# Performance work log

Measured on AMD Instinct MI355X. Metric: run time of the kernel, lower is better.

## Reference

```python
import jax, jax.numpy as jnp
import numpy as np

D_MODEL = 1024
NUM_HEADS = 16
D_K = D_MODEL // NUM_HEADS


def setup_inputs() -> dict:
    key = jax.random.key(0)
    ks = jax.random.split(key, 5)
    B, S = 4, 2048
    scale = 1.0 / np.sqrt(D_MODEL)
    x = jax.random.normal(ks[0], (B, S, D_MODEL), dtype=jnp.float32)
    Wq = jax.random.normal(ks[1], (D_MODEL, D_MODEL), dtype=jnp.float32) * scale
    Wk = jax.random.normal(ks[2], (D_MODEL, D_MODEL), dtype=jnp.float32) * scale
    Wv = jax.random.normal(ks[3], (D_MODEL, D_MODEL), dtype=jnp.float32) * scale
    Wo = jax.random.normal(ks[4], (D_MODEL, D_MODEL), dtype=jnp.float32) * scale
    return {"x": x, "Wq": Wq, "Wk": Wk, "Wv": Wv, "Wo": Wo}


def reference(x, Wq, Wk, Wv, Wo):
    B, S, _ = x.shape
    # projections (torch Linear: y = x @ W^T, no bias)
    def proj(W):
        y = jnp.einsum('bsd,ed->bse', x, W)
        # split heads: (b, s, h*dk) -> (b, h, s, dk)
        return y.reshape(B, S, NUM_HEADS, D_K).transpose(0, 2, 1, 3)
    Q, K, V = proj(Wq), proj(Wk), proj(Wv)
    scores = jnp.einsum('bhqd,bhkd->bhqk', Q, K) / np.sqrt(D_K)
    causal = jnp.tril(jnp.ones((S, S), dtype=bool))
    scores = jnp.where(causal, scores, -jnp.inf)
    attn = jax.nn.softmax(scores, axis=-1)
    out = jnp.einsum('bhqk,bhkd->bhqd', attn, V)
    out = out.transpose(0, 2, 1, 3).reshape(B, S, D_MODEL)
    return jnp.einsum('bse,de->bsd', out, Wo)
```

## Files before the change

kernel.cpp:

```cpp
#include <hip/hip_runtime.h>
#include <hip/hip_bf16.h>

typedef __attribute__((ext_vector_type(8))) short short8;
typedef __attribute__((ext_vector_type(4))) float f32x4;

static constexpr int DM = 1024;
static constexpr int NH = 16;
static constexpr int DK = 64;
static constexpr int SL = 2048;
static constexpr int BB = 4;
static constexpr size_t QKV_ELEMS = (size_t)BB * NH * SL * DK;
static constexpr float NEG_BIG = -30000.0f;
static constexpr float SC_LOG2E = 0.125f * 1.44269504088896340736f;

union PackB { __hip_bfloat16 h[8]; uint4 u; };
union Pack4 { __hip_bfloat16 h[4]; uint2 u; };

typedef __attribute__((address_space(1))) unsigned int gu32;
typedef __attribute__((address_space(3))) unsigned int lu32;
__device__ __forceinline__ void async_copy16(const void* g, void* l) {
    __builtin_amdgcn_global_load_lds((gu32*)g, (lu32*)l, 16, 0, 0);
}

__global__ __launch_bounds__(256)
void cvt_all(const float* __restrict__ x,
             const float* __restrict__ wq, const float* __restrict__ wk,
             const float* __restrict__ wv, const float* __restrict__ wo,
             __hip_bfloat16* __restrict__ dst)
{
    const size_t i = (size_t)blockIdx.x * 256 + threadIdx.x;
    const float* src; size_t local;
    if (i < 2097152) { src = x; local = i; }
    else {
        const size_t j = i - 2097152;
        const int r = (int)(j >> 18);
        local = j & 262143;
        src = (r == 0) ? wq : (r == 1) ? wk : (r == 2) ? wv : wo;
    }
    float4 f = reinterpret_cast<const float4*>(src)[local];
    Pack4 p;
    p.h[0] = __float2bfloat16(f.x); p.h[1] = __float2bfloat16(f.y);
    p.h[2] = __float2bfloat16(f.z); p.h[3] = __float2bfloat16(f.w);
    reinterpret_cast<uint2*>(dst)[i] = p.u;
}

__global__ __launch_bounds__(256)
void gemm_qkv(const __hip_bfloat16* __restrict__ A,
              const __hip_bfloat16* __restrict__ W,
              __hip_bfloat16* __restrict__ q_out,
              __hip_bfloat16* __restrict__ k_out,
              __hip_bfloat16* __restrict__ v_out)
{
    __shared__ __hip_bfloat16 As[128 * 32];
    __shared__ __hip_bfloat16 Bs[128 * 32];
    const int tid  = threadIdx.x;
    const int m0   = blockIdx.x * 128;
    const int n0   = blockIdx.y * 128;
    const int w    = tid >> 6;
    const int lane = tid & 63;
    const int quad = lane >> 4;
    const int ln   = lane & 15;
    const int wm   = (w & 1) * 64;
    const int wn   = (w >> 1) * 64;
    const int srow   = lane >> 2;
    const int schunk = (lane & 3) * 8;

    f32x4 acc[4][4] = {};

    for (int k0 = 0; k0 < DM; k0 += 32) {
        #pragma unroll
        for (int j = 0; j < 2; j++) {
            const int rbase = w * 32 + j * 16;
            async_copy16(A + (size_t)(m0 + rbase + srow) * DM + k0 + schunk,
                         &As[rbase * 32]);
            async_copy16(W + (size_t)(n0 + rbase + srow) * DM + k0 + schunk,
                         &Bs[rbase * 32]);
        }
        __syncthreads();

        short8 a[4], b[4];
        #pragma unroll
        for (int i = 0; i < 4; i++)
            a[i] = *reinterpret_cast<const short8*>(&As[(wm + i*16 + ln) * 32 + quad*8]);
        #pragma unroll
        for (int j = 0; j < 4; j++)
            b[j] = *reinterpret_cast<const short8*>(&Bs[(wn + j*16 + ln) * 32 + quad*8]);
        #pragma unroll
        for (int i = 0; i < 4; i++)
            #pragma unroll
            for (int j = 0; j < 4; j++)
                acc[i][j] = __builtin_amdgcn_mfma_f32_16x16x32_bf16(a[i], b[j], acc[i][j], 0, 0, 0);
        __syncthreads();
    }

    #pragma unroll
    for (int i = 0; i < 4; i++) {
        #pragma unroll
        for (int j = 0; j < 4; j++) {
            #pragma unroll
            for (int r = 0; r < 4; r++) {
                const int m = m0 + wm + i*16 + quad*4 + r;
                const int n = n0 + wn + j*16 + ln;
                const int b_ = m >> 11;
                const int s  = m & 2047;
                const int which = n >> 10;
                const int nn = n & 1023;
                const int h  = nn >> 6;
                const int d  = nn & 63;
                const __hip_bfloat16 v = __float2bfloat16(acc[i][j][r]);
                if (which == 0)
                    q_out[((size_t)((b_*NH + h)*SL + s))*DK + d] = v;
                else if (which == 1)
                    k_out[((size_t)((b_*NH + h)*SL + s))*DK + d] = v;
                else
                    v_out[((size_t)((b_*NH + h)*DK + d))*SL + s] = v;
            }
        }
    }
}

__global__ __launch_bounds__(256)
void gemm_wo(const __hip_bfloat16* __restrict__ A,
             const __hip_bfloat16* __restrict__ W,
             float* __restrict__ outp)
{
    __shared__ __hip_bfloat16 As[128 * 32];
    __shared__ __hip_bfloat16 Bs[128 * 32];
    const int tid  = threadIdx.x;
    const int m0   = blockIdx.x * 128;
    const int n0   = blockIdx.y * 128;
    const int w    = tid >> 6;
    const int lane = tid & 63;
    const int quad = lane >> 4;
    const int ln   = lane & 15;
    const int wm   = (w & 1) * 64;
    const int wn   = (w >> 1) * 64;
    const int srow   = lane >> 2;
    const int schunk = (lane & 3) * 8;

    f32x4 acc[4][4] = {};

    for (int k0 = 0; k0 < DM; k0 += 32) {
        #pragma unroll
        for (int j = 0; j < 2; j++) {
            const int rbase = w * 32 + j * 16;
            async_copy16(A + (size_t)(m0 + rbase + srow) * DM + k0 + schunk,
                         &As[rbase * 32]);
            async_copy16(W + (size_t)(n0 + rbase + srow) * DM + k0 + schunk,
                         &Bs[rbase * 32]);
        }
        __syncthreads();

        short8 a[4], b[4];
        #pragma unroll
        for (int i = 0; i < 4; i++)
            a[i] = *reinterpret_cast<const short8*>(&As[(wm + i*16 + ln) * 32 + quad*8]);
        #pragma unroll
        for (int j = 0; j < 4; j++)
            b[j] = *reinterpret_cast<const short8*>(&Bs[(wn + j*16 + ln) * 32 + quad*8]);
        #pragma unroll
        for (int i = 0; i < 4; i++)
            #pragma unroll
            for (int j = 0; j < 4; j++)
                acc[i][j] = __builtin_amdgcn_mfma_f32_16x16x32_bf16(a[i], b[j], acc[i][j], 0, 0, 0);
        __syncthreads();
    }

    #pragma unroll
    for (int i = 0; i < 4; i++)
        #pragma unroll
        for (int j = 0; j < 4; j++)
            #pragma unroll
            for (int r = 0; r < 4; r++) {
                const int m = m0 + wm + i*16 + quad*4 + r;
                const int n = n0 + wn + j*16 + ln;
                outp[(size_t)m * DM + n] = acc[i][j][r];
            }
}

template<bool A_BF16, int MODE>
__global__ __launch_bounds__(256)
void gemm_bt(const void* __restrict__ Ap,
             const float* __restrict__ W,
             void* __restrict__ outp)
{
    __shared__ __hip_bfloat16 As[128][40];
    __shared__ __hip_bfloat16 Bs[128][40];
    const int tid  = threadIdx.x;
    const int m0   = blockIdx.x * 128;
    const int n0   = blockIdx.y * 128;
    const int w    = tid >> 6;
    const int lane = tid & 63;
    const int quad = lane >> 4;
    const int ln   = lane & 15;
    const int wm   = (w & 1) * 64;
    const int wn   = (w >> 1) * 64;
    const int lr   = tid >> 1;
    const int lc   = (tid & 1) * 16;

    f32x4 acc[4][4] = {};

    for (int k0 = 0; k0 < DM; k0 += 32) {
        if (A_BF16) {
            const uint4* ap = reinterpret_cast<const uint4*>(
                (const __hip_bfloat16*)Ap + (size_t)(m0 + lr) * DM + k0 + lc);
            uint4 a0 = ap[0], a1 = ap[1];
            *reinterpret_cast<uint4*>(&As[lr][lc])     = a0;
            *reinterpret_cast<uint4*>(&As[lr][lc + 8]) = a1;
        } else {
            const float4* ap = reinterpret_cast<const float4*>(
                (const float*)Ap + (size_t)(m0 + lr) * DM + k0 + lc);
            float4 f0 = ap[0], f1 = ap[1], f2 = ap[2], f3 = ap[3];
            PackB p0, p1;
            p0.h[0] = __float2bfloat16(f0.x); p0.h[1] = __float2bfloat16(f0.y);
            p0.h[2] = __float2bfloat16(f0.z); p0.h[3] = __float2bfloat16(f0.w);
            p0.h[4] = __float2bfloat16(f1.x); p0.h[5] = __float2bfloat16(f1.y);
            p0.h[6] = __float2bfloat16(f1.z); p0.h[7] = __float2bfloat16(f1.w);
            p1.h[0] = __float2bfloat16(f2.x); p1.h[1] = __float2bfloat16(f2.y);
            p1.h[2] = __float2bfloat16(f2.z); p1.h[3] = __float2bfloat16(f2.w);
            p1.h[4] = __float2bfloat16(f3.x); p1.h[5] = __float2bfloat16(f3.y);
            p1.h[6] = __float2bfloat16(f3.z); p1.h[7] = __float2bfloat16(f3.w);
            *reinterpret_cast<uint4*>(&As[lr][lc])     = p0.u;
            *reinterpret_cast<uint4*>(&As[lr][lc + 8]) = p1.u;
        }
        {
            const float4* wp = reinterpret_cast<const float4*>(
                W + (size_t)(n0 + lr) * DM + k0 + lc);
            float4 f0 = wp[0], f1 = wp[1], f2 = wp[2], f3 = wp[3];
            PackB p0, p1;
            p0.h[0] = __float2bfloat16(f0.x); p0.h[1] = __float2bfloat16(f0.y);
            p0.h[2] = __float2bfloat16(f0.z); p0.h[3] = __float2bfloat16(f0.w);
            p0.h[4] = __float2bfloat16(f1.x); p0.h[5] = __float2bfloat16(f1.y);
            p0.h[6] = __float2bfloat16(f1.z); p0.h[7] = __float2bfloat16(f1.w);
            p1.h[0] = __float2bfloat16(f2.x); p1.h[1] = __float2bfloat16(f2.y);
            p1.h[2] = __float2bfloat16(f2.z); p1.h[3] = __float2bfloat16(f2.w);
            p1.h[4] = __float2bfloat16(f3.x); p1.h[5] = __float2bfloat16(f3.y);
            p1.h[6] = __float2bfloat16(f3.z); p1.h[7] = __float2bfloat16(f3.w);
            *reinterpret_cast<uint4*>(&Bs[lr][lc])     = p0.u;
            *reinterpret_cast<uint4*>(&Bs[lr][lc + 8]) = p1.u;
        }
        __syncthreads();

        short8 a[4], b[4];
        #pragma unroll
        for (int i = 0; i < 4; i++)
            a[i] = *reinterpret_cast<const short8*>(&As[wm + i*16 + ln][quad*8]);
        #pragma unroll
        for (int j = 0; j < 4; j++)
            b[j] = *reinterpret_cast<const short8*>(&Bs[wn + j*16 + ln][quad*8]);
        #pragma unroll
        for (int i = 0; i < 4; i++)
            #pragma unroll
            for (int j = 0; j < 4; j++)
                acc[i][j] = __builtin_amdgcn_mfma_f32_16x16x32_bf16(a[i], b[j], acc[i][j], 0, 0, 0);
        __syncthreads();
    }

    #pragma unroll
    for (int i = 0; i < 4; i++) {
        #pragma unroll
        for (int j = 0; j < 4; j++) {
            #pragma unroll
            for (int r = 0; r < 4; r++) {
                const int m = m0 + wm + i*16 + quad*4 + r;
                const int n = n0 + wn + j*16 + ln;
                const float v = acc[i][j][r];
                if (MODE == 2) {
                    ((float*)outp)[(size_t)m * DM + n] = v;
                } else {
                    const int b_ = m >> 11;
                    const int s  = m & 2047;
                    const int h  = n >> 6;
                    const int d  = n & 63;
                    size_t idx;
                    if (MODE == 0) idx = ((size_t)((b_*NH + h)*SL + s))*DK + d;
                    else           idx = ((size_t)((b_*NH + h)*DK + d))*SL + s;
                    ((__hip_bfloat16*)outp)[idx] = __float2bfloat16(v);
                }
            }
        }
    }
}

__global__ __launch_bounds__(256)
void attn_causal(const __hip_bfloat16* __restrict__ Q,
                 const __hip_bfloat16* __restrict__ K,
                 const __hip_bfloat16* __restrict__ Vt,
                 __hip_bfloat16* __restrict__ O)
{
    __shared__ __hip_bfloat16 Ks[64][72];
    __shared__ __hip_bfloat16 Vs[64][72];
    __shared__ __hip_bfloat16 p_lds[4][16][72];

    const int tid  = threadIdx.x;
    const int w    = tid >> 6;
    const int lane = tid & 63;
    const int quad = lane >> 4;
    const int ln   = lane & 15;
    const int bh   = blockIdx.y;
    const int b_   = bh >> 4;
    const int h    = bh & 15;

    const int srow   = tid >> 3;
    const int schunk = (tid & 7) * 8;

    const __hip_bfloat16* Qb = Q  + (size_t)bh * SL * DK;
    const __hip_bfloat16* Kb = K  + (size_t)bh * SL * DK;
    const __hip_bfloat16* Vb = Vt + (size_t)bh * DK * SL;

    for (int pass = 0; pass < 2; ++pass) {
        const int qt    = (pass == 0) ? (int)blockIdx.x : 31 - (int)blockIdx.x;
        const int q0    = qt * 64;
        const int qbase = q0 + w * 16;

        short8 aq0 = *reinterpret_cast<const short8*>(Qb + (size_t)(qbase + ln) * DK + quad*8);
        short8 aq1 = *reinterpret_cast<const short8*>(Qb + (size_t)(qbase + ln) * DK + 32 + quad*8);

        f32x4 acc[4] = {};
        float lsum[4] = {0.f, 0.f, 0.f, 0.f};

        for (int k0 = 0; k0 <= q0; k0 += 64) {
            const __hip_bfloat16* Kg = Kb + (size_t)(k0 + srow) * DK + schunk;
            uint4 kv0 = *reinterpret_cast<const uint4*>(Kg);
            uint4 kv1 = *reinterpret_cast<const uint4*>(Kg + 32 * DK);
            const __hip_bfloat16* Vg = Vb + (size_t)srow * SL + k0 + schunk;
            uint4 vv0 = *reinterpret_cast<const uint4*>(Vg);
            uint4 vv1 = *reinterpret_cast<const uint4*>(Vg + 32 * SL);
            __syncthreads();
            *reinterpret_cast<uint4*>(&Ks[srow     ][schunk]) = kv0;
            *reinterpret_cast<uint4*>(&Ks[srow + 32][schunk]) = kv1;
            *reinterpret_cast<uint4*>(&Vs[srow     ][schunk]) = vv0;
            *reinterpret_cast<uint4*>(&Vs[srow + 32][schunk]) = vv1;
            __syncthreads();

            f32x4 s[4];
            #pragma unroll
            for (int kc = 0; kc < 4; kc++) {
                short8 bk0 = *reinterpret_cast<const short8*>(&Ks[kc*16 + ln][quad*8]);
                short8 bk1 = *reinterpret_cast<const short8*>(&Ks[kc*16 + ln][32 + quad*8]);
                f32x4 z = {};
                z = __builtin_amdgcn_mfma_f32_16x16x32_bf16(aq0, bk0, z, 0, 0, 0);
                z = __builtin_amdgcn_mfma_f32_16x16x32_bf16(aq1, bk1, z, 0, 0, 0);
                s[kc] = z;
            }
            const bool diag = (k0 == q0);
            #pragma unroll
            for (int kc = 0; kc < 4; kc++) {
                #pragma unroll
                for (int r = 0; r < 4; r++) {
                    float v = s[kc][r] * SC_LOG2E;
                    if (diag) {
                        const int kg = k0 + kc*16 + ln;
                        const int qg = qbase + quad*4 + r;
                        if (kg > qg) v = NEG_BIG;
                    }
                    const float p = __builtin_amdgcn_exp2f(v);
                    lsum[r] += p;
                    p_lds[w][quad*4 + r][kc*16 + ln] = __float2bfloat16(p);
                }
            }
            short8 ap0 = *reinterpret_cast<const short8*>(&p_lds[w][ln][quad*8]);
            short8 ap1 = *reinterpret_cast<const short8*>(&p_lds[w][ln][32 + quad*8]);
            #pragma unroll
            for (int nt = 0; nt < 4; nt++) {
                short8 bv0 = *reinterpret_cast<const short8*>(&Vs[nt*16 + ln][quad*8]);
                short8 bv1 = *reinterpret_cast<const short8*>(&Vs[nt*16 + ln][32 + quad*8]);
                acc[nt] = __builtin_amdgcn_mfma_f32_16x16x32_bf16(ap0, bv0, acc[nt], 0, 0, 0);
                acc[nt] = __builtin_amdgcn_mfma_f32_16x16x32_bf16(ap1, bv1, acc[nt], 0, 0, 0);
            }
        }

        #pragma unroll
        for (int r = 0; r < 4; r++) {
            float v = lsum[r];
            v += __shfl_xor(v, 1, 64);
            v += __shfl_xor(v, 2, 64);
            v += __shfl_xor(v, 4, 64);
            v += __shfl_xor(v, 8, 64);
            lsum[r] = v;
        }

        #pragma unroll
        for (int nt = 0; nt < 4; nt++) {
            #pragma unroll
            for (int r = 0; r < 4; r++) {
                const int sI = qbase + quad*4 + r;
                const int d  = nt*16 + ln;
                const float v = acc[nt][r] / lsum[r];
                O[(((size_t)b_ * SL + sI) * NH + h) * DK + d] = __float2bfloat16(v);
            }
        }
    }
}

extern "C" void kernel_launch(void* const* d_in, const int* in_sizes, int n_in,
                              void* d_out, int out_size, void* d_ws, size_t ws_size,
                              hipStream_t stream)
{
    const float* x  = (const float*)d_in[0];
    const float* Wq = (const float*)d_in[1];
    const float* Wk = (const float*)d_in[2];
    const float* Wv = (const float*)d_in[3];
    const float* Wo = (const float*)d_in[4];

    __hip_bfloat16* q_ws = (__hip_bfloat16*)d_ws;
    __hip_bfloat16* k_ws = q_ws + QKV_ELEMS;
    __hip_bfloat16* v_ws = k_ws + QKV_ELEMS;

    const dim3 gb(256);
    const size_t FAST_WS = (3 * QKV_ELEMS + QKV_ELEMS + 4 * (size_t)DM * DM)
                           * sizeof(__hip_bfloat16);

    if (ws_size >= FAST_WS) {
        __hip_bfloat16* xb  = v_ws + QKV_ELEMS;
        __hip_bfloat16* wqb = xb  + QKV_ELEMS;
        __hip_bfloat16* wob = wqb + 3 * (size_t)DM * DM;

        cvt_all<<<12288, 256, 0, stream>>>(x, Wq, Wk, Wv, Wo, xb);

        gemm_qkv<<<dim3(64, 24), gb, 0, stream>>>(xb, wqb, q_ws, k_ws, v_ws);

        attn_causal<<<dim3(16, BB*NH), 256, 0, stream>>>(q_ws, k_ws, v_ws, xb);

        gemm_wo<<<dim3(64, 8), gb, 0, stream>>>(xb, wob, (float*)d_out);
    } else {
        __hip_bfloat16* obuf = (__hip_bfloat16*)d_out;
        float*          fbuf = (float*)d_ws;
        const dim3 gg(64, 8);
        gemm_bt<false, 0><<<gg, gb, 0, stream>>>(x, Wq, q_ws);
        gemm_bt<false, 0><<<gg, gb, 0, stream>>>(x, Wk, k_ws);
        gemm_bt<false, 1><<<gg, gb, 0, stream>>>(x, Wv, v_ws);
        attn_causal<<<dim3(16, BB*NH), 256, 0, stream>>>(q_ws, k_ws, v_ws, obuf);
        gemm_bt<true, 2><<<gg, gb, 0, stream>>>(obuf, Wo, fbuf);
        (void)hipMemcpyAsync(d_out, fbuf, QKV_ELEMS * sizeof(float),
                             hipMemcpyDeviceToDevice, stream);
    }
}
```

Measured before the change: 284.1 us.

## Widen GEMM K-tile with XOR-swizzled LDS and prefetch attention K/V tiles

The QKV and output-projection GEMMs now stage a 64-wide K slice per iteration into LDS using an XOR swizzle on the 16-byte chunk index, which halves the number of barriers and aims to avoid LDS bank conflicts on the MFMA fragment reads. The attention kernel register-prefetches the next K/V tile from global memory while the current tile is being computed, so load latency overlaps with MFMA work. It also raises wave priority around the MFMA sections with s_setprio. LDS use per GEMM block doubles and register pressure rises, which could lower occupancy.

```diff
diff --git a/kernel.cpp b/kernel.cpp
--- a/kernel.cpp
+++ b/kernel.cpp
@@ -51,8 +51,8 @@
               __hip_bfloat16* __restrict__ k_out,
               __hip_bfloat16* __restrict__ v_out)
 {
-    __shared__ __hip_bfloat16 As[128 * 32];
-    __shared__ __hip_bfloat16 Bs[128 * 32];
+    __shared__ __hip_bfloat16 As[128 * 64];
+    __shared__ __hip_bfloat16 Bs[128 * 64];
     const int tid  = threadIdx.x;
     const int m0   = blockIdx.x * 128;
     const int n0   = blockIdx.y * 128;
@@ -62,34 +62,39 @@
     const int ln   = lane & 15;
     const int wm   = (w & 1) * 64;
     const int wn   = (w >> 1) * 64;
-    const int srow   = lane >> 2;
-    const int schunk = (lane & 3) * 8;
+    const int srow = lane >> 3;
+    const int sch  = ((lane & 7) ^ srow) * 8;
 
     f32x4 acc[4][4] = {};
 
-    for (int k0 = 0; k0 < DM; k0 += 32) {
-        #pragma unroll
-        for (int j = 0; j < 2; j++) {
-            const int rbase = w * 32 + j * 16;
-            async_copy16(A + (size_t)(m0 + rbase + srow) * DM + k0 + schunk,
-                         &As[rbase * 32]);
-            async_copy16(W + (size_t)(n0 + rbase + srow) * DM + k0 + schunk,
-                         &Bs[rbase * 32]);
-        }
-        __syncthreads();
-
-        short8 a[4], b[4];
-        #pragma unroll
-        for (int i = 0; i < 4; i++)
-            a[i] = *reinterpret_cast<const short8*>(&As[(wm + i*16 + ln) * 32 + quad*8]);
-        #pragma unroll
-        for (int j = 0; j < 4; j++)
-            b[j] = *reinterpret_cast<const short8*>(&Bs[(wn + j*16 + ln) * 32 + quad*8]);
-        #pragma unroll
-        for (int i = 0; i < 4; i++)
+    for (int k0 = 0; k0 < DM; k0 += 64) {
+        #pragma unroll
+        for (int j = 0; j < 4; j++) {
+            const int rbase = w * 32 + j * 8;
+            async_copy16(A + (size_t)(m0 + rbase + srow) * DM + k0 + sch,
+                         &As[rbase * 64]);
+            async_copy16(W + (size_t)(n0 + rbase + srow) * DM + k0 + sch,
+                         &Bs[rbase * 64]);
+        }
+        __syncthreads();
+
+        #pragma unroll
+        for (int ks = 0; ks < 2; ks++) {
+            short8 a[4], b[4];
+            #pragma unroll
+            for (int i = 0; i < 4; i++)
+                a[i] = *reinterpret_cast<const short8*>(
+                    &As[(wm + i*16 + ln) * 64 + (((ks*4 + quad) ^ (ln & 7)) * 8)]);
             #pragma unroll
             for (int j = 0; j < 4; j++)
-                acc[i][j] = __builtin_amdgcn_mfma_f32_16x16x32_bf16(a[i], b[j], acc[i][j], 0, 0, 0);
+                b[j] = *reinterpret_cast<const short8*>(
+                    &Bs[(wn + j*16 + ln) * 64 + (((ks*4 + quad) ^ (ln & 7)) * 8)]);
+            #pragma unroll
+            for (int i = 0; i < 4; i++)
+                #pragma unroll
+                for (int j = 0; j < 4; j++)
+                    acc[i][j] = __builtin_amdgcn_mfma_f32_16x16x32_bf16(a[i], b[j], acc[i][j], 0, 0, 0);
+        }
         __syncthreads();
     }
 
@@ -124,8 +129,8 @@
              const __hip_bfloat16* __restrict__ W,
              float* __restrict__ outp)
 {
-    __shared__ __hip_bfloat16 As[128 * 32];
-    __shared__ __hip_bfloat16 Bs[128 * 32];
+    __shared__ __hip_bfloat16 As[128 * 64];
+    __shared__ __hip_bfloat16 Bs[128 * 64];
     const int tid  = threadIdx.x;
     const int m0   = blockIdx.x * 128;
     const int n0   = blockIdx.y * 128;
@@ -135,34 +140,39 @@
     const int ln   = lane & 15;
     const int wm   = (w & 1) * 64;
     const int wn   = (w >> 1) * 64;
-    const int srow   = lane >> 2;
-    const int schunk = (lane & 3) * 8;
+    const int srow = lane >> 3;
+    const int sch  = ((lane & 7) ^ srow) * 8;
 
     f32x4 acc[4][4] = {};
 
-    for (int k0 = 0; k0 < DM; k0 += 32) {
-        #pragma unroll
-        for (int j = 0; j < 2; j++) {
-            const int rbase = w * 32 + j * 16;
-            async_copy16(A + (size_t)(m0 + rbase + srow) * DM + k0 + schunk,
-                         &As[rbase * 32]);
-            async_copy16(W + (size_t)(n0 + rbase + srow) * DM + k0 + schunk,
-                         &Bs[rbase * 32]);
-        }
-        __syncthreads();
-
-        short8 a[4], b[4];
-        #pragma unroll
-        for (int i = 0; i < 4; i++)
-            a[i] = *reinterpret_cast<const short8*>(&As[(wm + i*16 + ln) * 32 + quad*8]);
-        #pragma unroll
-        for (int j = 0; j < 4; j++)
-            b[j] = *reinterpret_cast<const short8*>(&Bs[(wn + j*16 + ln) * 32 + quad*8]);
-        #pragma unroll
-        for (int i = 0; i < 4; i++)
+    for (int k0 = 0; k0 < DM; k0 += 64) {
+        #pragma unroll
+        for (int j = 0; j < 4; j++) {
+            const int rbase = w * 32 + j * 8;
+            async_copy16(A + (size_t)(m0 + rbase + srow) * DM + k0 + sch,
+                         &As[rbase * 64]);
+            async_copy16(W + (size_t)(n0 + rbase + srow) * DM + k0 + sch,
+                         &Bs[rbase * 64]);
+        }
+        __syncthreads();
+
+        #pragma unroll
+        for (int ks = 0; ks < 2; ks++) {
+            short8 a[4], b[4];
+            #pragma unroll
+            for (int i = 0; i < 4; i++)
+                a[i] = *reinterpret_cast<const short8*>(
+                    &As[(wm + i*16 + ln) * 64 + (((ks*4 + quad) ^ (ln & 7)) * 8)]);
             #pragma unroll
             for (int j = 0; j < 4; j++)
-                acc[i][j] = __builtin_amdgcn_mfma_f32_16x16x32_bf16(a[i], b[j], acc[i][j], 0, 0, 0);
+                b[j] = *reinterpret_cast<const short8*>(
+                    &Bs[(wn + j*16 + ln) * 64 + (((ks*4 + quad) ^ (ln & 7)) * 8)]);
+            #pragma unroll
+            for (int i = 0; i < 4; i++)
+                #pragma unroll
+                for (int j = 0; j < 4; j++)
+                    acc[i][j] = __builtin_amdgcn_mfma_f32_16x16x32_bf16(a[i], b[j], acc[i][j], 0, 0, 0);
+        }
         __syncthreads();
     }
 
@@ -319,13 +329,14 @@
         f32x4 acc[4] = {};
         float lsum[4] = {0.f, 0.f, 0.f, 0.f};
 
+        const __hip_bfloat16* Kg = Kb + (size_t)srow * DK + schunk;
+        const __hip_bfloat16* Vg = Vb + (size_t)srow * SL + schunk;
+        uint4 kv0 = *reinterpret_cast<const uint4*>(Kg);
+        uint4 kv1 = *reinterpret_cast<const uint4*>(Kg + 32 * DK);
+        uint4 vv0 = *reinterpret_cast<const uint4*>(Vg);
+        uint4 vv1 = *reinterpret_cast<const uint4*>(Vg + 32 * SL);
+
         for (int k0 = 0; k0 <= q0; k0 += 64) {
-            const __hip_bfloat16* Kg = Kb + (size_t)(k0 + srow) * DK + schunk;
-            uint4 kv0 = *reinterpret_cast<const uint4*>(Kg);
-            uint4 kv1 = *reinterpret_cast<const uint4*>(Kg + 32 * DK);
-            const __hip_bfloat16* Vg = Vb + (size_t)srow * SL + k0 + schunk;
-            uint4 vv0 = *reinterpret_cast<const uint4*>(Vg);
-            uint4 vv1 = *reinterpret_cast<const uint4*>(Vg + 32 * SL);
             __syncthreads();
             *reinterpret_cast<uint4*>(&Ks[srow     ][schunk]) = kv0;
             *reinterpret_cast<uint4*>(&Ks[srow + 32][schunk]) = kv1;
@@ -333,7 +344,17 @@
             *reinterpret_cast<uint4*>(&Vs[srow + 32][schunk]) = vv1;
             __syncthreads();
 
+            if (k0 + 64 <= q0) {
+                const __hip_bfloat16* Kg2 = Kb + (size_t)(k0 + 64 + srow) * DK + schunk;
+                const __hip_bfloat16* Vg2 = Vb + (size_t)srow * SL + (k0 + 64) + schunk;
+                kv0 = *reinterpret_cast<const uint4*>(Kg2);
+                kv1 = *reinterpret_cast<const uint4*>(Kg2 + 32 * DK);
+                vv0 = *reinterpret_cast<const uint4*>(Vg2);
+                vv1 = *reinterpret_cast<const uint4*>(Vg2 + 32 * SL);
+            }
+
             f32x4 s[4];
+            __builtin_amdgcn_s_setprio(1);
             #pragma unroll
             for (int kc = 0; kc < 4; kc++) {
                 short8 bk0 = *reinterpret_cast<const short8*>(&Ks[kc*16 + ln][quad*8]);
@@ -343,6 +364,7 @@
                 z = __builtin_amdgcn_mfma_f32_16x16x32_bf16(aq1, bk1, z, 0, 0, 0);
                 s[kc] = z;
             }
+            __builtin_amdgcn_s_setprio(0);
             const bool diag = (k0 == q0);
             #pragma unroll
             for (int kc = 0; kc < 4; kc++) {
@@ -361,6 +383,7 @@
             }
             short8 ap0 = *reinterpret_cast<const short8*>(&p_lds[w][ln][quad*8]);
             short8 ap1 = *reinterpret_cast<const short8*>(&p_lds[w][ln][32 + quad*8]);
+            __builtin_amdgcn_s_setprio(1);
             #pragma unroll
             for (int nt = 0; nt < 4; nt++) {
                 short8 bv0 = *reinterpret_cast<const short8*>(&Vs[nt*16 + ln][quad*8]);
@@ -368,6 +391,7 @@
                 acc[nt] = __builtin_amdgcn_mfma_f32_16x16x32_bf16(ap0, bv0, acc[nt], 0, 0, 0);
                 acc[nt] = __builtin_amdgcn_mfma_f32_16x16x32_bf16(ap1, bv1, acc[nt], 0, 0, 0);
             }
+            __builtin_amdgcn_s_setprio(0);
         }
 
         #pragma unroll
```

After: 296.1 us. 1.04x slower.
